# Performance work log

Hardware: AMD Instinct MI355X
Metric: run time of the kernel (lower is better)

Reference implementation:

```python
import jax, jax.numpy as jnp
import numpy as np

B, N, F_IN = 128, 2048, 17
D_NODE, GEMB, HEADS = 128, 32, 3
D_GAT = GEMB * HEADS   # 96
D_OUT = 256
LN_EPS = 1e-5
NEG_SLOPE = 0.2  # PyG GATv2Conv default leaky_relu slope


def layer_norm(x, g, b):
    mu = jnp.mean(x, axis=-1, keepdims=True)
    var = jnp.mean(jnp.square(x - mu), axis=-1, keepdims=True)
    return (x - mu) * jax.lax.rsqrt(var + LN_EPS) * g + b


def gelu(x):
    return jax.nn.gelu(x, approximate=False)  # torch nn.GELU default = exact erf


def gatv2_star(x, Wl, bl, Wr, br, att, bias):
    """GATv2Conv on the star graph: edges j->0 for all j, plus self-loops i->i.

    x: [B, N, F]. Node 0 aggregates over all N source nodes via softmax
    attention; every node i>0 only has its self-loop (alpha=1 -> out=xl[i]).
    """
    xl = (x @ Wl + bl).reshape(B, N, HEADS, GEMB)  # source transform
    xr = (x @ Wr + br).reshape(B, N, HEADS, GEMB)  # target transform
    # messages into node 0: e_j = a . leaky_relu(xl[j] + xr[0])
    e = jax.nn.leaky_relu(xl + xr[:, :1], negative_slope=NEG_SLOPE)  # [B,N,H,C]
    scores = jnp.einsum('bnhc,hc->bnh', e, att)                       # [B,N,H]
    alpha = jax.nn.softmax(scores, axis=1)
    out0 = jnp.einsum('bnh,bnhc->bhc', alpha, xl)                     # [B,H,C]
    out = xl.at[:, 0].set(out0)  # nodes i>0 keep xl[i] (single self-loop edge)
    return out.reshape(B, N, D_GAT) + bias


def setup_inputs() -> dict:
    key = jax.random.key(0)
    ks = jax.random.split(key, 16)
    f32 = jnp.float32

    def w(k, shape, scale=0.1):
        return (jax.random.normal(k, shape, dtype=f32) * scale)

    return {
        'inputs': jax.random.normal(ks[0], (B, N * F_IN), dtype=f32),
        # fc_node + norm
        'W_node': w(ks[1], (F_IN, D_NODE)), 'b_node': jnp.zeros((D_NODE,), f32),
        'lnn_g': jnp.ones((D_NODE,), f32), 'lnn_b': jnp.zeros((D_NODE,), f32),
        # conv1 (GATv2: lin_l, lin_r, att, bias)
        'Wl1': w(ks[2], (D_NODE, D_GAT)), 'bl1': jnp.zeros((D_GAT,), f32),
        'Wr1': w(ks[3], (D_NODE, D_GAT)), 'br1': jnp.zeros((D_GAT,), f32),
        'att1': w(ks[4], (HEADS, GEMB)), 'bias1': jnp.zeros((D_GAT,), f32),
        'lnc1_g': jnp.ones((D_GAT,), f32), 'lnc1_b': jnp.zeros((D_GAT,), f32),
        # conv2
        'Wl2': w(ks[5], (D_GAT, D_GAT)), 'bl2': jnp.zeros((D_GAT,), f32),
        'Wr2': w(ks[6], (D_GAT, D_GAT)), 'br2': jnp.zeros((D_GAT,), f32),
        'att2': w(ks[7], (HEADS, GEMB)), 'bias2': jnp.zeros((D_GAT,), f32),
        'lnc2_g': jnp.ones((D_GAT,), f32), 'lnc2_b': jnp.zeros((D_GAT,), f32),
        # SoftmaxAggregation temperature (learnable, init 1)
        't': jnp.ones((), f32),
        # fc_out + norm
        'W_out': w(ks[8], (D_GAT, D_OUT)), 'b_out': jnp.zeros((D_OUT,), f32),
        'lno_g': jnp.ones((D_OUT,), f32), 'lno_b': jnp.zeros((D_OUT,), f32),
    }


def reference(inputs, W_node, b_node, lnn_g, lnn_b,
              Wl1, bl1, Wr1, br1, att1, bias1, lnc1_g, lnc1_b,
              Wl2, bl2, Wr2, br2, att2, bias2, lnc2_g, lnc2_b,
              t, W_out, b_out, lno_g, lno_b):
    x = inputs.reshape(B, N, F_IN)
    # local=False -> no feature masking
    x = layer_norm(gelu(x @ W_node + b_node), lnn_g, lnn_b)            # [B,N,128]
    x = layer_norm(gelu(gatv2_star(x, Wl1, bl1, Wr1, br1, att1, bias1)), lnc1_g, lnc1_b)
    x = layer_norm(gelu(gatv2_star(x, Wl2, bl2, Wr2, br2, att2, bias2)), lnc2_g, lnc2_b)
    # SoftmaxAggregation(t, learn=True): per-graph, per-channel softmax weights
    w = jax.nn.softmax(t * x, axis=1)
    pooled = jnp.sum(w * x, axis=1)                                    # [B,96]
    out = layer_norm(gelu(pooled @ W_out + b_out), lno_g, lno_b)        # [B,256]
    return out
```

## Files before the change

kernel.cpp:

```cpp
#include <hip/hip_runtime.h>
#include <hip/hip_bf16.h>
#include <math.h>

#define BB 128
#define NN 2048
#define FIN 17

#define SCALE_I 1048576.0f
#define INV_SCALE 9.5367431640625e-07f

typedef unsigned short ushort_t;
typedef unsigned long long ull_t;
typedef __attribute__((ext_vector_type(4))) unsigned short u16x4;
typedef __attribute__((ext_vector_type(8))) short s16x8;
typedef __attribute__((ext_vector_type(4))) float f32x4;

__device__ __forceinline__ float b2f(unsigned short u) {
    unsigned int v = ((unsigned int)u) << 16;
    return __builtin_bit_cast(float, v);
}
__device__ __forceinline__ unsigned short f2b(float f) {
    __hip_bfloat16 h = __float2bfloat16(f);
    return __builtin_bit_cast(unsigned short, h);
}
__device__ __forceinline__ unsigned short f2b_fast(float f) {
    unsigned int u = __builtin_bit_cast(unsigned int, f);
    u += 0x7FFFu + ((u >> 16) & 1u);
    return (unsigned short)(u >> 16);
}
__device__ __forceinline__ float gelu_f(float x) {
    float ax = fabsf(x) * 0.70710678118654752f;
    float t = 1.0f / (1.0f + 0.3275911f * ax);
    float poly = t * (0.254829592f +
                 t * (-0.284496736f +
                 t * (1.421413741f +
                 t * (-1.453152027f +
                 t * 1.061405429f))));
    float erfv = 1.0f - poly * __expf(-ax * ax);
    erfv = (x >= 0.f) ? erfv : -erfv;
    return 0.5f * x * (1.0f + erfv);
}
__device__ __forceinline__ float lrelu_f(float x) {
    return x >= 0.0f ? x : 0.2f * x;
}
__device__ __forceinline__ ull_t q20(float x) {
    return (ull_t)(long long)(x * SCALE_I);
}

__global__ __launch_bounds__(256) void k_zero64(ull_t* __restrict__ p, int n) {
    int i = blockIdx.x * 256 + threadIdx.x;
    if (i < n) p[i] = 0ull;
}

__global__ __launch_bounds__(256) void k_fcnode(
    const float* __restrict__ X, const float* __restrict__ W,
    const float* __restrict__ bias, const float* __restrict__ g,
    const float* __restrict__ beta, ushort_t* __restrict__ out) {
    __shared__ float Ws[FIN * 128];
    __shared__ float xs[64 * FIN];
    __shared__ float bl[128], gl[128], bet[128];
    int tid = threadIdx.x;
    long long rbase = (long long)blockIdx.x * 64;
    for (int i = tid; i < FIN * 128; i += 256) Ws[i] = W[i];
    for (int i = tid; i < 64 * FIN; i += 256) xs[i] = X[rbase * FIN + i];
    if (tid < 128) {
        bl[tid] = bias[tid]; gl[tid] = g[tid]; bet[tid] = beta[tid];
    }
    __syncthreads();
    int lane32 = tid & 31, sub = tid >> 5;
    int c0 = 4 * lane32;
    f32x4 acc[8] = {};
#pragma unroll
    for (int k = 0; k < FIN; k++) {
        f32x4 w = *(const f32x4*)(Ws + k * 128 + c0);
#pragma unroll
        for (int r = 0; r < 8; r++) {
            float xv = xs[(sub + 8 * r) * FIN + k];
            acc[r][0] = fmaf(xv, w[0], acc[r][0]);
            acc[r][1] = fmaf(xv, w[1], acc[r][1]);
            acc[r][2] = fmaf(xv, w[2], acc[r][2]);
            acc[r][3] = fmaf(xv, w[3], acc[r][3]);
        }
    }
#pragma unroll
    for (int r = 0; r < 8; r++) {
        int lr = sub + 8 * r;
        float v[4], s = 0.f, sq = 0.f;
#pragma unroll
        for (int j = 0; j < 4; j++) {
            v[j] = gelu_f(acc[r][j] + bl[c0 + j]);
            s += v[j]; sq += v[j] * v[j];
        }
#pragma unroll
        for (int mk = 16; mk >= 1; mk >>= 1) {
            s += __shfl_xor(s, mk, 32); sq += __shfl_xor(sq, mk, 32);
        }
        float mean = s * (1.f / 128.f);
        float var = sq * (1.f / 128.f) - mean * mean;
        float rstd = rsqrtf(var + 1e-5f);
        u16x4 o4;
#pragma unroll
        for (int j = 0; j < 4; j++)
            o4[j] = f2b_fast((v[j] - mean) * rstd * gl[c0 + j] + bet[c0 + j]);
        *(u16x4*)(out + (rbase + lr) * 128 + c0) = o4;
    }
}

template <int K>
__global__ __launch_bounds__(256) void k_wprep(
    const float* __restrict__ W, ushort_t* __restrict__ hi, ushort_t* __restrict__ lo) {
    constexpr int S = K / 32;
    int gid = blockIdx.x * 256 + threadIdx.x;
    if (gid >= 6 * S * 64) return;
    int lane = gid & 63, f = gid >> 6;
    int t = f / S, s = f - t * S;
    int n = 16 * t + (lane & 15);
    int kbase = 32 * s + 8 * (lane >> 4);
#pragma unroll
    for (int j = 0; j < 8; j++) {
        float w = W[(kbase + j) * 96 + n];
        ushort_t h = f2b(w);
        float rem = w - b2f(h);
        hi[gid * 8 + j] = h;
        lo[gid * 8 + j] = f2b(rem);
    }
}

template <int K>
__global__ __launch_bounds__(128) void k_xr0(
    const ushort_t* __restrict__ X, const float* __restrict__ Wr,
    const float* __restrict__ br, float* __restrict__ xr0) {
    int b = blockIdx.x, c = threadIdx.x;
    __shared__ float xs[K];
    if (threadIdx.x < K) xs[threadIdx.x] = b2f(X[(long long)b * NN * K + threadIdx.x]);
    __syncthreads();
    if (c >= 96) return;
    float acc = br[c];
    for (int k = 0; k < K; k++) acc = fmaf(xs[k], Wr[k * 96 + c], acc);
    xr0[b * 96 + c] = acc;
}

template <int K, bool POOLF>
__global__ __launch_bounds__(256) void k_conv(
    const ushort_t* __restrict__ X,
    const ushort_t* __restrict__ Whi, const ushort_t* __restrict__ Wlo,
    const float* __restrict__ bl, const float* __restrict__ att,
    const float* __restrict__ xr0,
    const float* __restrict__ bias, const float* __restrict__ lng,
    const float* __restrict__ lnb,
    ull_t* __restrict__ w0acc,
    ull_t* __restrict__ zacc,
    ushort_t* __restrict__ Xout,
    ull_t* __restrict__ pacc,
    const float* __restrict__ tptr)
{
    constexpr int S = K / 32;
    constexpr int NFRAG = 6 * S * 64;
    __shared__ s16x8 lWh[NFRAG];
    __shared__ s16x8 lWl[NFRAG];
    int tid = threadIdx.x;
    {
        const s16x8* gh = (const s16x8*)Whi;
        const s16x8* gl8 = (const s16x8*)Wlo;
        for (int i = tid; i < NFRAG; i += 256) {
            lWh[i] = gh[i];
            lWl[i] = gl8[i];
        }
    }
    __syncthreads();

    int wave = tid >> 6, lane = tid & 63;
    int hi4 = lane >> 4, cl = lane & 15;
    int row0 = blockIdx.x * 128 + wave * 32;
    int b = row0 >> 11;

    f32x4 acc[2][6] = {};
#pragma unroll
    for (int s = 0; s < S; s++) {
        s16x8 a0 = *(const s16x8*)(X + (size_t)(row0 + cl) * K + s * 32 + hi4 * 8);
        s16x8 a1 = *(const s16x8*)(X + (size_t)(row0 + 16 + cl) * K + s * 32 + hi4 * 8);
#pragma unroll
        for (int t = 0; t < 6; t++) {
            s16x8 bh = lWh[(t * S + s) * 64 + lane];
            s16x8 bo = lWl[(t * S + s) * 64 + lane];
            acc[0][t] = __builtin_amdgcn_mfma_f32_16x16x32_bf16(a0, bh, acc[0][t], 0, 0, 0);
            acc[0][t] = __builtin_amdgcn_mfma_f32_16x16x32_bf16(a0, bo, acc[0][t], 0, 0, 0);
            acc[1][t] = __builtin_amdgcn_mfma_f32_16x16x32_bf16(a1, bh, acc[1][t], 0, 0, 0);
            acc[1][t] = __builtin_amdgcn_mfma_f32_16x16x32_bf16(a1, bo, acc[1][t], 0, 0, 0);
        }
    }

    float blc[6], xrc[6], attc[6], bic[6], gc[6], bcc[6];
#pragma unroll
    for (int t = 0; t < 6; t++) {
        int c = 16 * t + cl;
        blc[t] = bl[c]; xrc[t] = xr0[b * 96 + c]; attc[t] = att[c];
        bic[t] = bias[c]; gc[t] = lng[c]; bcc[t] = lnb[c];
    }
    float tv = POOLF ? tptr[0] : 0.f;

    float w0p[6] = {0.f, 0.f, 0.f, 0.f, 0.f, 0.f};
    float zp[3] = {0.f, 0.f, 0.f};
    float psp[6] = {0.f, 0.f, 0.f, 0.f, 0.f, 0.f};
    float pwp[6] = {0.f, 0.f, 0.f, 0.f, 0.f, 0.f};

#pragma unroll
    for (int q = 0; q < 2; q++) {
#pragma unroll
        for (int i = 0; i < 4; i++) {
            int row = row0 + q * 16 + hi4 * 4 + i;
            float xl[6];
#pragma unroll
            for (int t = 0; t < 6; t++) xl[t] = acc[q][t][i] + blc[t];
            float pv[6];
#pragma unroll
            for (int t = 0; t < 6; t++) pv[t] = attc[t] * lrelu_f(xl[t] + xrc[t]);
            float p0 = pv[0] + pv[1], p1 = pv[2] + pv[3], p2 = pv[4] + pv[5];
            float o[6], s = 0.f, sq = 0.f;
#pragma unroll
            for (int t = 0; t < 6; t++) {
                o[t] = gelu_f(xl[t] + bic[t]);
                s += o[t]; sq += o[t] * o[t];
            }
#pragma unroll
            for (int mk = 1; mk <= 8; mk <<= 1) {
                p0 += __shfl_xor(p0, mk, 64);
                p1 += __shfl_xor(p1, mk, 64);
                p2 += __shfl_xor(p2, mk, 64);
                s  += __shfl_xor(s,  mk, 64);
                sq += __shfl_xor(sq, mk, 64);
            }
            float e0 = __expf(fminf(p0, 24.f));
            float e1 = __expf(fminf(p1, 24.f));
            float e2 = __expf(fminf(p2, 24.f));
            w0p[0] = fmaf(e0, xl[0], w0p[0]); w0p[1] = fmaf(e0, xl[1], w0p[1]);
            w0p[2] = fmaf(e1, xl[2], w0p[2]); w0p[3] = fmaf(e1, xl[3], w0p[3]);
            w0p[4] = fmaf(e2, xl[4], w0p[4]); w0p[5] = fmaf(e2, xl[5], w0p[5]);
            zp[0] += e0; zp[1] += e1; zp[2] += e2;
            float mean = s * (1.f / 96.f);
            float var = sq * (1.f / 96.f) - mean * mean;
            float rstd = rsqrtf(var + 1e-5f);
            if ((row & (NN - 1)) != 0) {
                if (!POOLF) {
#pragma unroll
                    for (int t = 0; t < 6; t++)
                        Xout[(size_t)row * 96 + 16 * t + cl] =
                            f2b_fast((o[t] - mean) * rstd * gc[t] + bcc[t]);
                } else {
#pragma unroll
                    for (int t = 0; t < 6; t++) {
                        float v = (o[t] - mean) * rstd * gc[t] + bcc[t];
                        float pe = __expf(fminf(tv * v, 24.f));
                        psp[t] += pe;
                        pwp[t] = fmaf(pe, v, pwp[t]);
                    }
                }
            }
        }
    }

#pragma unroll
    for (int t = 0; t < 6; t++) {
        w0p[t] += __shfl_xor(w0p[t], 16, 64);
        w0p[t] += __shfl_xor(w0p[t], 32, 64);
    }
#pragma unroll
    for (int h = 0; h < 3; h++) {
        zp[h] += __shfl_xor(zp[h], 16, 64);
        zp[h] += __shfl_xor(zp[h], 32, 64);
    }
    if (POOLF) {
#pragma unroll
        for (int t = 0; t < 6; t++) {
            psp[t] += __shfl_xor(psp[t], 16, 64);
            psp[t] += __shfl_xor(psp[t], 32, 64);
            pwp[t] += __shfl_xor(pwp[t], 16, 64);
            pwp[t] += __shfl_xor(pwp[t], 32, 64);
        }
    }
    if (lane < 16) {
#pragma unroll
        for (int t = 0; t < 6; t++)
            atomicAdd(w0acc + b * 96 + 16 * t + lane, q20(w0p[t]));
        if (POOLF) {
#pragma unroll
            for (int t = 0; t < 6; t++) {
                atomicAdd(pacc + b * 192 + 16 * t + lane, q20(psp[t]));
                atomicAdd(pacc + b * 192 + 96 + 16 * t + lane, q20(pwp[t]));
            }
        }
    }
    if (lane == 0) {
        atomicAdd(zacc + b * 4 + 0, q20(zp[0]));
        atomicAdd(zacc + b * 4 + 1, q20(zp[1]));
        atomicAdd(zacc + b * 4 + 2, q20(zp[2]));
    }
}

template <int LAYER>
__global__ __launch_bounds__(128) void k_row0(
    const ull_t* __restrict__ w0acc, const ull_t* __restrict__ zacc,
    const float* __restrict__ bias, const float* __restrict__ g,
    const float* __restrict__ beta, ushort_t* __restrict__ X2,
    float* __restrict__ row0v) {
    int b = blockIdx.x, t = threadIdx.x;
    __shared__ float vv[96];
    __shared__ float red2[2];
    float val = 0.f;
    if (t < 96) {
        float wf = (float)(long long)w0acc[b * 96 + t];
        float zf = (float)(long long)zacc[b * 4 + (t >> 5)];
        float out0 = wf / zf;
        val = gelu_f(out0 + bias[t]);
        vv[t] = val;
    }
    __syncthreads();
    if (t < 32) {
        float a = vv[t], b2 = vv[t + 32], c = vv[t + 64];
        float s = a + b2 + c, sq = a * a + b2 * b2 + c * c;
#pragma unroll
        for (int mk = 16; mk >= 1; mk >>= 1) { s += __shfl_xor(s, mk, 32); sq += __shfl_xor(sq, mk, 32); }
        if (t == 0) { red2[0] = s; red2[1] = sq; }
    }
    __syncthreads();
    float mean = red2[0] * (1.f / 96.f);
    float var = red2[1] * (1.f / 96.f) - mean * mean;
    float rstd = rsqrtf(var + 1e-5f);
    if (t < 96) {
        float ln = (val - mean) * rstd * g[t] + beta[t];
        if (LAYER == 1) {
            X2[(long long)b * NN * 96 + t] = f2b(ln);
        } else {
            row0v[b * 96 + t] = ln;
        }
    }
}

__global__ __launch_bounds__(256) void k_out(
    const ull_t* __restrict__ pacc, const float* __restrict__ row0v,
    const float* __restrict__ tptr, const float* __restrict__ W,
    const float* __restrict__ bias, const float* __restrict__ g,
    const float* __restrict__ beta, float* __restrict__ out) {
    int b = blockIdx.x, c = threadIdx.x;
    __shared__ float ps[96];
    __shared__ float rs[4], rq[4];
    if (c < 96) {
        float ln0 = row0v[b * 96 + c];
        float pe0 = __expf(fminf(tptr[0] * ln0, 24.f));
        float S = (float)(long long)pacc[b * 192 + c] * INV_SCALE + pe0;
        float Wp = (float)(long long)pacc[b * 192 + 96 + c] * INV_SCALE + pe0 * ln0;
        ps[c] = Wp / S;
    }
    __syncthreads();
    float acc = bias[c];
    for (int k = 0; k < 96; k++) acc = fmaf(ps[k], W[k * 256 + c], acc);
    float v = gelu_f(acc);
    float s = v, sq = v * v;
#pragma unroll
    for (int mk = 32; mk >= 1; mk >>= 1) { s += __shfl_xor(s, mk, 64); sq += __shfl_xor(sq, mk, 64); }
    if ((c & 63) == 0) { rs[c >> 6] = s; rq[c >> 6] = sq; }
    __syncthreads();
    s = rs[0] + rs[1] + rs[2] + rs[3];
    sq = rq[0] + rq[1] + rq[2] + rq[3];
    float mean = s * (1.f / 256.f);
    float var = sq * (1.f / 256.f) - mean * mean;
    float rstd = rsqrtf(var + 1e-5f);
    out[b * 256 + c] = (v - mean) * rstd * g[c] + beta[c];
}

extern "C" void kernel_launch(void* const* d_in, const int* in_sizes, int n_in,
                              void* d_out, int out_size, void* d_ws, size_t ws_size,
                              hipStream_t stream) {
    const float* in0    = (const float*)d_in[0];
    const float* W_node = (const float*)d_in[1];
    const float* b_node = (const float*)d_in[2];
    const float* lnn_g  = (const float*)d_in[3];
    const float* lnn_b  = (const float*)d_in[4];
    const float* Wl1 = (const float*)d_in[5];
    const float* bl1 = (const float*)d_in[6];
    const float* Wr1 = (const float*)d_in[7];
    const float* br1 = (const float*)d_in[8];
    const float* att1 = (const float*)d_in[9];
    const float* bias1 = (const float*)d_in[10];
    const float* lnc1_g = (const float*)d_in[11];
    const float* lnc1_b = (const float*)d_in[12];
    const float* Wl2 = (const float*)d_in[13];
    const float* bl2 = (const float*)d_in[14];
    const float* Wr2 = (const float*)d_in[15];
    const float* br2 = (const float*)d_in[16];
    const float* att2 = (const float*)d_in[17];
    const float* bias2 = (const float*)d_in[18];
    const float* lnc2_g = (const float*)d_in[19];
    const float* lnc2_b = (const float*)d_in[20];
    const float* tptr = (const float*)d_in[21];
    const float* W_out = (const float*)d_in[22];
    const float* b_out = (const float*)d_in[23];
    const float* lno_g = (const float*)d_in[24];
    const float* lno_b = (const float*)d_in[25];

    auto alignup = [](size_t x) { return (x + 255) & ~(size_t)255; };

    const size_t wf1 = (size_t)6 * 4 * 64 * 8;
    const size_t wf2 = (size_t)6 * 3 * 64 * 8;
    char* base = (char*)d_ws;
    ushort_t* wf1h = (ushort_t*)base;             base += alignup(wf1 * 2);
    ushort_t* wf1l = (ushort_t*)base;             base += alignup(wf1 * 2);
    ushort_t* wf2h = (ushort_t*)base;             base += alignup(wf2 * 2);
    ushort_t* wf2l = (ushort_t*)base;             base += alignup(wf2 * 2);
    size_t fixed = (size_t)(base - (char*)d_ws);

    auto need = [&](int bcx) -> size_t {
        size_t rn = (size_t)bcx * NN;
        return fixed
             + alignup(rn * 128 * 2)
             + alignup(rn * 96 * 2)
             + alignup((size_t)bcx * 96 * 4)
             + alignup((size_t)bcx * 392 * 8)
             + alignup((size_t)bcx * 96 * 4);
    };
    int bc = BB;
    while (bc > 1 && need(bc) > ws_size) bc >>= 1;

    k_wprep<128><<<6, 256, 0, stream>>>(Wl1, wf1h, wf1l);
    k_wprep<96><<<5, 256, 0, stream>>>(Wl2, wf2h, wf2l);

    for (int cb = 0; cb < BB; cb += bc) {
        size_t rn = (size_t)bc * NN;
        char* p = base;
        ushort_t* Xbuf  = (ushort_t*)p; p += alignup(rn * 128 * 2);
        ushort_t* X2buf = (ushort_t*)p; p += alignup(rn * 96 * 2);
        float*    xr0b  = (float*)p;    p += alignup((size_t)bc * 96 * 4);
        ull_t*    accs  = (ull_t*)p;    p += alignup((size_t)bc * 392 * 8);
        float*    row0v = (float*)p;
        ull_t* w0a1 = accs;
        ull_t* za1  = w0a1 + (size_t)bc * 96;
        ull_t* w0a2 = za1 + (size_t)bc * 4;
        ull_t* za2  = w0a2 + (size_t)bc * 96;
        ull_t* pacc = za2 + (size_t)bc * 4;

        const float* inC = in0 + (size_t)cb * NN * FIN;
        float* outC = (float*)d_out + (size_t)cb * 256;
        int nz = bc * 392;

        k_zero64<<<(nz + 255) / 256, 256, 0, stream>>>(accs, nz);
        k_fcnode<<<bc * NN / 64, 256, 0, stream>>>(inC, W_node, b_node, lnn_g, lnn_b, Xbuf);

        k_xr0<128><<<bc, 128, 0, stream>>>(Xbuf, Wr1, br1, xr0b);
        k_conv<128, false><<<bc * NN / 128, 256, 0, stream>>>(
            Xbuf, wf1h, wf1l, bl1, att1, xr0b, bias1, lnc1_g, lnc1_b,
            w0a1, za1, X2buf, nullptr, nullptr);
        k_row0<1><<<bc, 128, 0, stream>>>(w0a1, za1, bias1, lnc1_g, lnc1_b,
                                          X2buf, nullptr);

        k_xr0<96><<<bc, 128, 0, stream>>>(X2buf, Wr2, br2, xr0b);
        k_conv<96, true><<<bc * NN / 128, 256, 0, stream>>>(
            X2buf, wf2h, wf2l, bl2, att2, xr0b, bias2, lnc2_g, lnc2_b,
            w0a2, za2, nullptr, pacc, tptr);
        k_row0<2><<<bc, 128, 0, stream>>>(w0a2, za2, bias2, lnc2_g, lnc2_b,
                                          nullptr, row0v);

        k_out<<<bc, 256, 0, stream>>>(pacc, row0v, tptr, W_out, b_out,
                                      lno_g, lno_b, outC);
    }
}
```

Measured before the change: 236.3 us.

## Fuse xr0/row0 kernels into neighbors and transpose MFMA output layout in conv

Removes the two k_xr0 launches and the layer-2 k_row0 launch. The target-node transforms are now computed inside k_fcnode (layer 1) and k_row0x (layer 2), and the row-0 finalisation moves into k_out. In k_conv the MFMA operands are swapped so each lane holds one row with 4 contiguous channels. This turns the per-row epilogue into vectorised stores and moves the cross-lane reductions from per-row to the end. Per-channel parameters are staged in shared memory, and the A fragments are loaded up front. The cost is more registers and more shuffles at the end for the accumulated sums.

```diff
diff --git a/kernel.cpp b/kernel.cpp
--- a/kernel.cpp
+++ b/kernel.cpp
@@ -55,10 +55,13 @@
 __global__ __launch_bounds__(256) void k_fcnode(
     const float* __restrict__ X, const float* __restrict__ W,
     const float* __restrict__ bias, const float* __restrict__ g,
-    const float* __restrict__ beta, ushort_t* __restrict__ out) {
+    const float* __restrict__ beta, ushort_t* __restrict__ out,
+    const float* __restrict__ Wr1, const float* __restrict__ br1,
+    float* __restrict__ xr0out) {
     __shared__ float Ws[FIN * 128];
     __shared__ float xs[64 * FIN];
     __shared__ float bl[128], gl[128], bet[128];
+    __shared__ float x0row[128];
     int tid = threadIdx.x;
     long long rbase = (long long)blockIdx.x * 64;
     for (int i = tid; i < FIN * 128; i += 256) Ws[i] = W[i];
@@ -100,9 +103,20 @@
         float rstd = rsqrtf(var + 1e-5f);
         u16x4 o4;
 #pragma unroll
-        for (int j = 0; j < 4; j++)
-            o4[j] = f2b_fast((v[j] - mean) * rstd * gl[c0 + j] + bet[c0 + j]);
+        for (int j = 0; j < 4; j++) {
+            float fin = (v[j] - mean) * rstd * gl[c0 + j] + bet[c0 + j];
+            o4[j] = f2b_fast(fin);
+            if (r == 0 && sub == 0) x0row[c0 + j] = fin;
+        }
         *(u16x4*)(out + (rbase + lr) * 128 + c0) = o4;
+    }
+    __syncthreads();
+    if ((blockIdx.x & 31) == 0 && tid < 96) {
+        float a = br1[tid];
+#pragma unroll 8
+        for (int k = 0; k < 128; k++)
+            a = fmaf(x0row[k], Wr1[k * 96 + tid], a);
+        xr0out[(blockIdx.x >> 5) * 96 + tid] = a;
     }
 }
 
@@ -124,20 +138,6 @@
         hi[gid * 8 + j] = h;
         lo[gid * 8 + j] = f2b(rem);
     }
-}
-
-template <int K>
-__global__ __launch_bounds__(128) void k_xr0(
-    const ushort_t* __restrict__ X, const float* __restrict__ Wr,
-    const float* __restrict__ br, float* __restrict__ xr0) {
-    int b = blockIdx.x, c = threadIdx.x;
-    __shared__ float xs[K];
-    if (threadIdx.x < K) xs[threadIdx.x] = b2f(X[(long long)b * NN * K + threadIdx.x]);
-    __syncthreads();
-    if (c >= 96) return;
-    float acc = br[c];
-    for (int k = 0; k < K; k++) acc = fmaf(xs[k], Wr[k * 96 + c], acc);
-    xr0[b * 96 + c] = acc;
 }
 
 template <int K, bool POOLF>
@@ -158,7 +158,9 @@
     constexpr int NFRAG = 6 * S * 64;
     __shared__ s16x8 lWh[NFRAG];
     __shared__ s16x8 lWl[NFRAG];
+    __shared__ float prm[6][96];
     int tid = threadIdx.x;
+    int b = (blockIdx.x * 128) >> 11;
     {
         const s16x8* gh = (const s16x8*)Whi;
         const s16x8* gl8 = (const s16x8*)Wlo;
@@ -166,93 +168,117 @@
             lWh[i] = gh[i];
             lWl[i] = gl8[i];
         }
+        if (tid < 96) {
+            prm[0][tid] = bl[tid];
+            prm[1][tid] = xr0[b * 96 + tid];
+            prm[2][tid] = att[tid];
+            prm[3][tid] = bias[tid];
+            prm[4][tid] = lng[tid];
+            prm[5][tid] = lnb[tid];
+        }
     }
     __syncthreads();
 
     int wave = tid >> 6, lane = tid & 63;
     int hi4 = lane >> 4, cl = lane & 15;
     int row0 = blockIdx.x * 128 + wave * 32;
-    int b = row0 >> 11;
-
+
+    s16x8 a0[S], a1[S];
+#pragma unroll
+    for (int s = 0; s < S; s++) {
+        a0[s] = *(const s16x8*)(X + (size_t)(row0 + cl) * K + s * 32 + hi4 * 8);
+        a1[s] = *(const s16x8*)(X + (size_t)(row0 + 16 + cl) * K + s * 32 + hi4 * 8);
+    }
     f32x4 acc[2][6] = {};
 #pragma unroll
     for (int s = 0; s < S; s++) {
-        s16x8 a0 = *(const s16x8*)(X + (size_t)(row0 + cl) * K + s * 32 + hi4 * 8);
-        s16x8 a1 = *(const s16x8*)(X + (size_t)(row0 + 16 + cl) * K + s * 32 + hi4 * 8);
 #pragma unroll
         for (int t = 0; t < 6; t++) {
             s16x8 bh = lWh[(t * S + s) * 64 + lane];
             s16x8 bo = lWl[(t * S + s) * 64 + lane];
-            acc[0][t] = __builtin_amdgcn_mfma_f32_16x16x32_bf16(a0, bh, acc[0][t], 0, 0, 0);
-            acc[0][t] = __builtin_amdgcn_mfma_f32_16x16x32_bf16(a0, bo, acc[0][t], 0, 0, 0);
-            acc[1][t] = __builtin_amdgcn_mfma_f32_16x16x32_bf16(a1, bh, acc[1][t], 0, 0, 0);
-            acc[1][t] = __builtin_amdgcn_mfma_f32_16x16x32_bf16(a1, bo, acc[1][t], 0, 0, 0);
-        }
-    }
-
-    float blc[6], xrc[6], attc[6], bic[6], gc[6], bcc[6];
-#pragma unroll
-    for (int t = 0; t < 6; t++) {
-        int c = 16 * t + cl;
-        blc[t] = bl[c]; xrc[t] = xr0[b * 96 + c]; attc[t] = att[c];
-        bic[t] = bias[c]; gc[t] = lng[c]; bcc[t] = lnb[c];
-    }
+            acc[0][t] = __builtin_amdgcn_mfma_f32_16x16x32_bf16(bh, a0[s], acc[0][t], 0, 0, 0);
+            acc[0][t] = __builtin_amdgcn_mfma_f32_16x16x32_bf16(bo, a0[s], acc[0][t], 0, 0, 0);
+            acc[1][t] = __builtin_amdgcn_mfma_f32_16x16x32_bf16(bh, a1[s], acc[1][t], 0, 0, 0);
+            acc[1][t] = __builtin_amdgcn_mfma_f32_16x16x32_bf16(bo, a1[s], acc[1][t], 0, 0, 0);
+        }
+    }
+
     float tv = POOLF ? tptr[0] : 0.f;
-
-    float w0p[6] = {0.f, 0.f, 0.f, 0.f, 0.f, 0.f};
+    f32x4 w0p[6] = {};
     float zp[3] = {0.f, 0.f, 0.f};
-    float psp[6] = {0.f, 0.f, 0.f, 0.f, 0.f, 0.f};
-    float pwp[6] = {0.f, 0.f, 0.f, 0.f, 0.f, 0.f};
+    f32x4 psp[6] = {};
+    f32x4 pwp[6] = {};
 
 #pragma unroll
     for (int q = 0; q < 2; q++) {
-#pragma unroll
-        for (int i = 0; i < 4; i++) {
-            int row = row0 + q * 16 + hi4 * 4 + i;
-            float xl[6];
-#pragma unroll
-            for (int t = 0; t < 6; t++) xl[t] = acc[q][t][i] + blc[t];
-            float pv[6];
-#pragma unroll
-            for (int t = 0; t < 6; t++) pv[t] = attc[t] * lrelu_f(xl[t] + xrc[t]);
-            float p0 = pv[0] + pv[1], p1 = pv[2] + pv[3], p2 = pv[4] + pv[5];
-            float o[6], s = 0.f, sq = 0.f;
-#pragma unroll
-            for (int t = 0; t < 6; t++) {
-                o[t] = gelu_f(xl[t] + bic[t]);
-                s += o[t]; sq += o[t] * o[t];
+        int row = row0 + q * 16 + cl;
+        float xl[6][4], o[6][4];
+        float p0 = 0.f, p1 = 0.f, p2 = 0.f, s = 0.f, sq = 0.f;
+#pragma unroll
+        for (int t = 0; t < 6; t++) {
+            int c = 16 * t + hi4 * 4;
+            f32x4 blv = *(const f32x4*)&prm[0][c];
+            f32x4 xrv = *(const f32x4*)&prm[1][c];
+            f32x4 atv = *(const f32x4*)&prm[2][c];
+            f32x4 biv = *(const f32x4*)&prm[3][c];
+#pragma unroll
+            for (int i = 0; i < 4; i++) {
+                float x = acc[q][t][i] + blv[i];
+                xl[t][i] = x;
+                float pc = atv[i] * lrelu_f(x + xrv[i]);
+                if ((t >> 1) == 0) p0 += pc; else if ((t >> 1) == 1) p1 += pc; else p2 += pc;
+                float ov = gelu_f(x + biv[i]);
+                o[t][i] = ov;
+                s += ov; sq += ov * ov;
             }
-#pragma unroll
-            for (int mk = 1; mk <= 8; mk <<= 1) {
-                p0 += __shfl_xor(p0, mk, 64);
-                p1 += __shfl_xor(p1, mk, 64);
-                p2 += __shfl_xor(p2, mk, 64);
-                s  += __shfl_xor(s,  mk, 64);
-                sq += __shfl_xor(sq, mk, 64);
-            }
-            float e0 = __expf(fminf(p0, 24.f));
-            float e1 = __expf(fminf(p1, 24.f));
-            float e2 = __expf(fminf(p2, 24.f));
-            w0p[0] = fmaf(e0, xl[0], w0p[0]); w0p[1] = fmaf(e0, xl[1], w0p[1]);
-            w0p[2] = fmaf(e1, xl[2], w0p[2]); w0p[3] = fmaf(e1, xl[3], w0p[3]);
-            w0p[4] = fmaf(e2, xl[4], w0p[4]); w0p[5] = fmaf(e2, xl[5], w0p[5]);
-            zp[0] += e0; zp[1] += e1; zp[2] += e2;
-            float mean = s * (1.f / 96.f);
-            float var = sq * (1.f / 96.f) - mean * mean;
-            float rstd = rsqrtf(var + 1e-5f);
-            if ((row & (NN - 1)) != 0) {
-                if (!POOLF) {
-#pragma unroll
-                    for (int t = 0; t < 6; t++)
-                        Xout[(size_t)row * 96 + 16 * t + cl] =
-                            f2b_fast((o[t] - mean) * rstd * gc[t] + bcc[t]);
-                } else {
-#pragma unroll
-                    for (int t = 0; t < 6; t++) {
-                        float v = (o[t] - mean) * rstd * gc[t] + bcc[t];
+        }
+#pragma unroll
+        for (int mk = 16; mk <= 32; mk <<= 1) {
+            p0 += __shfl_xor(p0, mk, 64);
+            p1 += __shfl_xor(p1, mk, 64);
+            p2 += __shfl_xor(p2, mk, 64);
+            s  += __shfl_xor(s,  mk, 64);
+            sq += __shfl_xor(sq, mk, 64);
+        }
+        float e0 = __expf(fminf(p0, 24.f));
+        float e1 = __expf(fminf(p1, 24.f));
+        float e2 = __expf(fminf(p2, 24.f));
+#pragma unroll
+        for (int t = 0; t < 6; t++) {
+            float eh = (t >> 1) == 0 ? e0 : ((t >> 1) == 1 ? e1 : e2);
+#pragma unroll
+            for (int i = 0; i < 4; i++)
+                w0p[t][i] = fmaf(eh, xl[t][i], w0p[t][i]);
+        }
+        zp[0] += e0; zp[1] += e1; zp[2] += e2;
+        float mean = s * (1.f / 96.f);
+        float var = sq * (1.f / 96.f) - mean * mean;
+        float rstd = rsqrtf(var + 1e-5f);
+        if ((row & (NN - 1)) != 0) {
+            if (!POOLF) {
+#pragma unroll
+                for (int t = 0; t < 6; t++) {
+                    int c = 16 * t + hi4 * 4;
+                    f32x4 gv = *(const f32x4*)&prm[4][c];
+                    f32x4 bev = *(const f32x4*)&prm[5][c];
+                    u16x4 o4;
+#pragma unroll
+                    for (int i = 0; i < 4; i++)
+                        o4[i] = f2b_fast((o[t][i] - mean) * rstd * gv[i] + bev[i]);
+                    *(u16x4*)(Xout + (size_t)row * 96 + c) = o4;
+                }
+            } else {
+#pragma unroll
+                for (int t = 0; t < 6; t++) {
+                    int c = 16 * t + hi4 * 4;
+                    f32x4 gv = *(const f32x4*)&prm[4][c];
+                    f32x4 bev = *(const f32x4*)&prm[5][c];
+#pragma unroll
+                    for (int i = 0; i < 4; i++) {
+                        float v = (o[t][i] - mean) * rstd * gv[i] + bev[i];
                         float pe = __expf(fminf(tv * v, 24.f));
-                        psp[t] += pe;
-                        pwp[t] = fmaf(pe, v, pwp[t]);
+                        psp[t][i] += pe;
+                        pwp[t][i] = fmaf(pe, v, pwp[t][i]);
                     }
                 }
             }
@@ -260,35 +286,40 @@
     }
 
 #pragma unroll
-    for (int t = 0; t < 6; t++) {
-        w0p[t] += __shfl_xor(w0p[t], 16, 64);
-        w0p[t] += __shfl_xor(w0p[t], 32, 64);
-    }
-#pragma unroll
-    for (int h = 0; h < 3; h++) {
-        zp[h] += __shfl_xor(zp[h], 16, 64);
-        zp[h] += __shfl_xor(zp[h], 32, 64);
-    }
+    for (int t = 0; t < 6; t++)
+#pragma unroll
+        for (int i = 0; i < 4; i++)
+#pragma unroll
+            for (int mk = 1; mk <= 8; mk <<= 1)
+                w0p[t][i] += __shfl_xor(w0p[t][i], mk, 64);
+#pragma unroll
+    for (int h = 0; h < 3; h++)
+#pragma unroll
+        for (int mk = 1; mk <= 8; mk <<= 1)
+            zp[h] += __shfl_xor(zp[h], mk, 64);
     if (POOLF) {
 #pragma unroll
-        for (int t = 0; t < 6; t++) {
-            psp[t] += __shfl_xor(psp[t], 16, 64);
-            psp[t] += __shfl_xor(psp[t], 32, 64);
-            pwp[t] += __shfl_xor(pwp[t], 16, 64);
-            pwp[t] += __shfl_xor(pwp[t], 32, 64);
-        }
-    }
-    if (lane < 16) {
-#pragma unroll
         for (int t = 0; t < 6; t++)
-            atomicAdd(w0acc + b * 96 + 16 * t + lane, q20(w0p[t]));
-        if (POOLF) {
-#pragma unroll
-            for (int t = 0; t < 6; t++) {
-                atomicAdd(pacc + b * 192 + 16 * t + lane, q20(psp[t]));
-                atomicAdd(pacc + b * 192 + 96 + 16 * t + lane, q20(pwp[t]));
+#pragma unroll
+            for (int i = 0; i < 4; i++)
+#pragma unroll
+                for (int mk = 1; mk <= 8; mk <<= 1) {
+                    psp[t][i] += __shfl_xor(psp[t][i], mk, 64);
+                    pwp[t][i] += __shfl_xor(pwp[t][i], mk, 64);
+                }
+    }
+    if (cl == 0) {
+#pragma unroll
+        for (int t = 0; t < 6; t++)
+#pragma unroll
+            for (int i = 0; i < 4; i++) {
+                int c = 16 * t + hi4 * 4 + i;
+                atomicAdd(w0acc + b * 96 + c, q20(w0p[t][i]));
+                if (POOLF) {
+                    atomicAdd(pacc + b * 192 + c, q20(psp[t][i]));
+                    atomicAdd(pacc + b * 192 + 96 + c, q20(pwp[t][i]));
+                }
             }
-        }
     }
     if (lane == 0) {
         atomicAdd(zacc + b * 4 + 0, q20(zp[0]));
@@ -297,21 +328,20 @@
     }
 }
 
-template <int LAYER>
-__global__ __launch_bounds__(128) void k_row0(
+__global__ __launch_bounds__(128) void k_row0x(
     const ull_t* __restrict__ w0acc, const ull_t* __restrict__ zacc,
     const float* __restrict__ bias, const float* __restrict__ g,
     const float* __restrict__ beta, ushort_t* __restrict__ X2,
-    float* __restrict__ row0v) {
+    const float* __restrict__ Wr2, const float* __restrict__ br2,
+    float* __restrict__ xr0out) {
     int b = blockIdx.x, t = threadIdx.x;
-    __shared__ float vv[96];
+    __shared__ float vv[96], lnS[96];
     __shared__ float red2[2];
     float val = 0.f;
     if (t < 96) {
         float wf = (float)(long long)w0acc[b * 96 + t];
         float zf = (float)(long long)zacc[b * 4 + (t >> 5)];
-        float out0 = wf / zf;
-        val = gelu_f(out0 + bias[t]);
+        val = gelu_f(wf / zf + bias[t]);
         vv[t] = val;
     }
     __syncthreads();
@@ -328,28 +358,57 @@
     float rstd = rsqrtf(var + 1e-5f);
     if (t < 96) {
         float ln = (val - mean) * rstd * g[t] + beta[t];
-        if (LAYER == 1) {
-            X2[(long long)b * NN * 96 + t] = f2b(ln);
-        } else {
-            row0v[b * 96 + t] = ln;
-        }
+        X2[(long long)b * NN * 96 + t] = f2b(ln);
+        lnS[t] = ln;
+    }
+    __syncthreads();
+    if (t < 96) {
+        float a = br2[t];
+#pragma unroll 8
+        for (int k = 0; k < 96; k++)
+            a = fmaf(lnS[k], Wr2[k * 96 + t], a);
+        xr0out[b * 96 + t] = a;
     }
 }
 
 __global__ __launch_bounds__(256) void k_out(
-    const ull_t* __restrict__ pacc, const float* __restrict__ row0v,
+    const ull_t* __restrict__ w0acc, const ull_t* __restrict__ zacc,
+    const ull_t* __restrict__ pacc, const float* __restrict__ bias2,
+    const float* __restrict__ g2, const float* __restrict__ be2,
     const float* __restrict__ tptr, const float* __restrict__ W,
     const float* __restrict__ bias, const float* __restrict__ g,
     const float* __restrict__ beta, float* __restrict__ out) {
     int b = blockIdx.x, c = threadIdx.x;
-    __shared__ float ps[96];
+    __shared__ float vv[96], ps[96];
+    __shared__ float red2[2];
     __shared__ float rs[4], rq[4];
+    float val = 0.f;
     if (c < 96) {
-        float ln0 = row0v[b * 96 + c];
-        float pe0 = __expf(fminf(tptr[0] * ln0, 24.f));
-        float S = (float)(long long)pacc[b * 192 + c] * INV_SCALE + pe0;
-        float Wp = (float)(long long)pacc[b * 192 + 96 + c] * INV_SCALE + pe0 * ln0;
-        ps[c] = Wp / S;
+        float wf = (float)(long long)w0acc[b * 96 + c];
+        float zf = (float)(long long)zacc[b * 4 + (c >> 5)];
+        val = gelu_f(wf / zf + bias2[c]);
+        vv[c] = val;
+    }
+    __syncthreads();
+    if (c < 32) {
+        float a = vv[c], b2 = vv[c + 32], c3 = vv[c + 64];
+        float s = a + b2 + c3, sq = a * a + b2 * b2 + c3 * c3;
+#pragma unroll
+        for (int mk = 16; mk >= 1; mk >>= 1) { s += __shfl_xor(s, mk, 32); sq += __shfl_xor(sq, mk, 32); }
+        if (c == 0) { red2[0] = s; red2[1] = sq; }
+    }
+    __syncthreads();
+    {
+        float mean0 = red2[0] * (1.f / 96.f);
+        float var0 = red2[1] * (1.f / 96.f) - mean0 * mean0;
+        float rstd0 = rsqrtf(var0 + 1e-5f);
+        if (c < 96) {
+            float ln0 = (val - mean0) * rstd0 * g2[c] + be2[c];
+            float pe0 = __expf(fminf(tptr[0] * ln0, 24.f));
+            float S = (float)(long long)pacc[b * 192 + c] * INV_SCALE + pe0;
+            float Wp = (float)(long long)pacc[b * 192 + 96 + c] * INV_SCALE + pe0 * ln0;
+            ps[c] = Wp / S;
+        }
     }
     __syncthreads();
     float acc = bias[c];
@@ -415,8 +474,7 @@
              + alignup(rn * 128 * 2)
              + alignup(rn * 96 * 2)
              + alignup((size_t)bcx * 96 * 4)
-             + alignup((size_t)bcx * 392 * 8)
-             + alignup((size_t)bcx * 96 * 4);
+             + alignup((size_t)bcx * 392 * 8);
     };
     int bc = BB;
     while (bc > 1 && need(bc) > ws_size) bc >>= 1;
@@ -430,8 +488,7 @@
         ushort_t* Xbuf  = (ushort_t*)p; p += alignup(rn * 128 * 2);
         ushort_t* X2buf = (ushort_t*)p; p += alignup(rn * 96 * 2);
         float*    xr0b  = (float*)p;    p += alignup((size_t)bc * 96 * 4);
-        ull_t*    accs  = (ull_t*)p;    p += alignup((size_t)bc * 392 * 8);
-        float*    row0v = (float*)p;
+        ull_t*    accs  = (ull_t*)p;
         ull_t* w0a1 = accs;
         ull_t* za1  = w0a1 + (size_t)bc * 96;
         ull_t* w0a2 = za1 + (size_t)bc * 4;
@@ -443,23 +500,17 @@
         int nz = bc * 392;
 
         k_zero64<<<(nz + 255) / 256, 256, 0, stream>>>(accs, nz);
-        k_fcnode<<<bc * NN / 64, 256, 0, stream>>>(inC, W_node, b_node, lnn_g, lnn_b, Xbuf);
-
-        k_xr0<128><<<bc, 128, 0, stream>>>(Xbuf, Wr1, br1, xr0b);
+        k_fcnode<<<bc * NN / 64, 256, 0, stream>>>(inC, W_node, b_node, lnn_g, lnn_b,
+                                                   Xbuf, Wr1, br1, xr0b);
         k_conv<128, false><<<bc * NN / 128, 256, 0, stream>>>(
             Xbuf, wf1h, wf1l, bl1, att1, xr0b, bias1, lnc1_g, lnc1_b,
             w0a1, za1, X2buf, nullptr, nullptr);
-        k_row0<1><<<bc, 128, 0, stream>>>(w0a1, za1, bias1, lnc1_g, lnc1_b,
-                                          X2buf, nullptr);
-
-        k_xr0<96><<<bc, 128, 0, stream>>>(X2buf, Wr2, br2, xr0b);
+        k_row0x<<<bc, 128, 0, stream>>>(w0a1, za1, bias1, lnc1_g, lnc1_b,
+                                        X2buf, Wr2, br2, xr0b);
         k_conv<96, true><<<bc * NN / 128, 256, 0, stream>>>(
             X2buf, wf2h, wf2l, bl2, att2, xr0b, bias2, lnc2_g, lnc2_b,
             w0a2, za2, nullptr, pacc, tptr);
-        k_row0<2><<<bc, 128, 0, stream>>>(w0a2, za2, bias2, lnc2_g, lnc2_b,
-                                          nullptr, row0v);
-
-        k_out<<<bc, 256, 0, stream>>>(pacc, row0v, tptr, W_out, b_out,
-                                      lno_g, lno_b, outC);
-    }
-}
+        k_out<<<bc, 256, 0, stream>>>(w0a2, za2, pacc, bias2, lnc2_g, lnc2_b,
+                                      tptr, W_out, b_out, lno_g, lno_b, outC);
+    }
+}
```

After: 306.0 us. 29.5% more time.
